# Optimization experiments

Measured on AMD Instinct MI355X. Metric: run time of the kernel, lower is better.

Reference implementation:

```python
import jax, jax.numpy as jnp
import numpy as np

B, T, NH, EX, VOCAB, NLAYER = 8, 510, 12, 768, 256, 6
NBLK = 2 * NLAYER - 1          # 11 blocks, all with out=ex
NE = T + 2                     # CustomEmb output dim = n_embd = 512
HD = EX // NH
EXIT_SCALE = 1.0 / float(np.sqrt(4 * NBLK))  # torch init divides 'exit' params by sqrt(#exit params)


def _ln(x, s, b):
    m = jnp.mean(x, axis=-1, keepdims=True)
    v = jnp.mean((x - m) ** 2, axis=-1, keepdims=True)
    return (x - m) * jax.lax.rsqrt(v + 1e-5) * s + b


def setup_inputs() -> dict:
    key = jax.random.key(0)
    ks = iter(jax.random.split(key, 40))
    def n(shape, scale=0.02):
        return jax.random.normal(next(ks), shape, jnp.float32) * scale
    inp = {}
    inp['idx'] = jax.random.randint(next(ks), (B, T), 0, 2)
    inp['lin_w'] = n((NE, EX)); inp['lin_b'] = n((EX,))
    # stacked per-block params (leading dim NBLK), torch Linear math y = x @ W + b with W stored (in,out)
    inp['ln1_s'] = jnp.ones((NBLK, EX), jnp.float32); inp['ln1_b'] = jnp.zeros((NBLK, EX), jnp.float32)
    inp['qw'] = n((NBLK, EX, EX)); inp['qb'] = n((NBLK, EX))
    inp['kw'] = n((NBLK, EX, EX)); inp['kb'] = n((NBLK, EX))
    inp['vw'] = n((NBLK, EX, EX)); inp['vb'] = n((NBLK, EX))
    inp['ew'] = n((NBLK, EX, EX)) * EXIT_SCALE; inp['eb'] = n((NBLK, EX)) * EXIT_SCALE
    inp['ln2_s'] = jnp.ones((NBLK, EX), jnp.float32); inp['ln2_b'] = jnp.zeros((NBLK, EX), jnp.float32)
    inp['m1w'] = n((NBLK, EX, 4 * EX)); inp['m1b'] = n((NBLK, 4 * EX))
    inp['m2w'] = n((NBLK, 4 * EX, EX)) * EXIT_SCALE; inp['m2b'] = n((NBLK, EX)) * EXIT_SCALE
    inp['lnf_s'] = jnp.ones((EX,), jnp.float32); inp['lnf_b'] = jnp.zeros((EX,), jnp.float32)
    inp['head_w'] = n((EX * T, VOCAB)); inp['head_b'] = n((VOCAB,))
    return inp


def reference(idx, lin_w, lin_b, ln1_s, ln1_b, qw, qb, kw, kb, vw, vb, ew, eb,
              ln2_s, ln2_b, m1w, m1b, m2w, m2b, lnf_s, lnf_b, head_w, head_b):
    # CustomEmb: one-hot of binary token + identity positional encoding -> [B,T,T+2]
    e0 = (idx == 0).astype(jnp.float32)
    e1 = (idx == 1).astype(jnp.float32)
    pos = jnp.broadcast_to(jnp.eye(T, dtype=jnp.float32), (B, T, T))
    x = jnp.concatenate([e0[:, :, None], e1[:, :, None], pos], axis=2)
    x = jax.nn.relu(x @ lin_w + lin_b)                       # [B,T,EX]
    mask = jnp.tril(jnp.ones((T, T), bool))
    inv_sqrt_d = 1.0 / float(np.sqrt(HD))

    def block(x, p):
        l1s, l1b, Qw, Qb, Kw, Kb, Vw, Vb, Ew, Eb, l2s, l2b, M1w, M1b, M2w, M2b = p
        h = _ln(x, l1s, l1b)
        q = (h @ Qw + Qb).reshape(B, T, NH, HD)
        k = (h @ Kw + Kb).reshape(B, T, NH, HD)
        v = (h @ Vw + Vb).reshape(B, T, NH, HD)
        att = jnp.einsum('bqhd,bkhd->bhqk', q, k) * inv_sqrt_d
        att = jnp.where(mask, att, -jnp.inf)
        probs = jax.nn.softmax(att, axis=-1)
        y = jnp.einsum('bhqk,bkhd->bqhd', probs, v).reshape(B, T, EX)
        x = x + y @ Ew + Eb
        h2 = _ln(x, l2s, l2b)
        x = x + jax.nn.relu(h2 @ M1w + M1b) @ M2w + M2b      # MLP depth=2: initial+relu+exit
        return x, None

    x, _ = jax.lax.scan(block, x, (ln1_s, ln1_b, qw, qb, kw, kb, vw, vb,
                                   ew, eb, ln2_s, ln2_b, m1w, m1b, m2w, m2b))
    x = _ln(x, lnf_s, lnf_b)
    return x.reshape(B, -1) @ head_w + head_b                # [B, VOCAB]
```

## Files before the change

### kernel.cpp

```cpp
#include <hip/hip_runtime.h>
#include <hip/hip_bf16.h>
#include <math.h>

constexpr int cB = 8, cT = 510, cNH = 12, cEX = 768, cVOC = 256, cNBLK = 11, cHD = 64;
constexpr int cMB = 512;
constexpr int cMP = 4096;
constexpr int cQKV = 3 * cEX;

typedef __attribute__((ext_vector_type(8))) short bf16x8;
typedef __attribute__((ext_vector_type(4))) float f32x4;
using bf16 = __hip_bfloat16;

__device__ inline void gload16(const void* g, void* l) {
    __builtin_amdgcn_global_load_lds((const __attribute__((address_space(1))) unsigned int*)g,
                                     (__attribute__((address_space(3))) unsigned int*)l, 16, 0, 0);
}
__device__ inline short f2bs(float f) {
    bf16 b = __float2bfloat16(f);
    return *reinterpret_cast<short*>(&b);
}

__global__ __launch_bounds__(256) void embed_kernel(
    const int* __restrict__ idx, const float* __restrict__ lin_w,
    const float* __restrict__ lin_b, float* __restrict__ x)
{
    int row = blockIdx.x;
    int b = row >> 9, t = row & 511;
    float* xr = x + (size_t)row * cEX;
    if (t >= cT) {
        for (int j = threadIdx.x; j < cEX; j += 256) xr[j] = 0.0f;
        return;
    }
    int tok = idx[b * cT + t] & 1;
    const float* wt = lin_w + (size_t)tok * cEX;
    const float* wp = lin_w + (size_t)(2 + t) * cEX;
    for (int j = threadIdx.x; j < cEX; j += 256) {
        float val = wt[j] + wp[j] + lin_b[j];
        xr[j] = fmaxf(val, 0.0f);
    }
}

template<typename OUT>
__global__ __launch_bounds__(256) void ln_wave(
    const float* __restrict__ in, const float* __restrict__ s,
    const float* __restrict__ bsh, OUT* __restrict__ out)
{
    const int wid = threadIdx.x >> 6, lane = threadIdx.x & 63;
    const int row = blockIdx.x * 4 + wid;
    const float* xr = in + (size_t)row * cEX;
    float4 v[3];
    float sum = 0.f, sq = 0.f;
#pragma unroll
    for (int p = 0; p < 3; ++p) {
        v[p] = *(const float4*)&xr[p * 256 + lane * 4];
        sum += v[p].x + v[p].y + v[p].z + v[p].w;
        sq  += v[p].x * v[p].x + v[p].y * v[p].y + v[p].z * v[p].z + v[p].w * v[p].w;
    }
#pragma unroll
    for (int off = 1; off < 64; off <<= 1) {
        sum += __shfl_xor(sum, off, 64);
        sq  += __shfl_xor(sq, off, 64);
    }
    float mean = sum * (1.0f / cEX);
    float var = sq * (1.0f / cEX) - mean * mean;
    float rstd = rsqrtf(var + 1e-5f);
    OUT* outr = out + (size_t)row * cEX;
#pragma unroll
    for (int p = 0; p < 3; ++p) {
        int c = p * 256 + lane * 4;
        float4 sv = *(const float4*)&s[c];
        float4 bv = *(const float4*)&bsh[c];
        float o0 = (v[p].x - mean) * rstd * sv.x + bv.x;
        float o1 = (v[p].y - mean) * rstd * sv.y + bv.y;
        float o2 = (v[p].z - mean) * rstd * sv.z + bv.z;
        float o3 = (v[p].w - mean) * rstd * sv.w + bv.w;
        if constexpr (sizeof(OUT) == 2) {
            short4 pk;
            pk.x = f2bs(o0); pk.y = f2bs(o1); pk.z = f2bs(o2); pk.w = f2bs(o3);
            *(short4*)&outr[c] = pk;
        } else {
            *(float4*)&outr[c] = make_float4(o0, o1, o2, o3);
        }
    }
}

__global__ __launch_bounds__(256) void transpose_w(
    const float* __restrict__ W, bf16* __restrict__ WT,
    int K, int N, size_t w_stride, size_t wt_stride, int wt_row_off)
{
    __shared__ float t[32][33];
    const float* Wb = W + (size_t)blockIdx.z * w_stride;
    bf16* WTb = WT + (size_t)blockIdx.z * wt_stride;
    int n0 = blockIdx.x * 32, k0 = blockIdx.y * 32;
    int c = threadIdx.x & 31, ty = threadIdx.x >> 5;
#pragma unroll
    for (int it = 0; it < 4; ++it) {
        int r = ty + it * 8;
        t[r][c] = Wb[(size_t)(k0 + r) * N + n0 + c];
    }
    __syncthreads();
#pragma unroll
    for (int it = 0; it < 4; ++it) {
        int a = ty + it * 8;
        WTb[(size_t)(wt_row_off + n0 + a) * K + k0 + c] = __float2bfloat16(t[c][a]);
    }
}

__global__ __launch_bounds__(256) void concat_bias(
    const float* __restrict__ qb, const float* __restrict__ kb,
    const float* __restrict__ vb, float* __restrict__ qkvb)
{
    int i = blockIdx.x * 256 + threadIdx.x;
    if (i >= cNBLK * cQKV) return;
    int blk = i / cQKV, c = i - blk * cQKV;
    const float* src; int cc = c;
    if (c < cEX)            { src = qb; }
    else if (c < 2 * cEX)   { src = kb; cc = c - cEX; }
    else                    { src = vb; cc = c - 2 * cEX; }
    qkvb[i] = src[(size_t)blk * cEX + cc];
}

template<int FM, int FN, bool RELU, bool RESID, bool OUTBF16, bool VT>
__global__ __launch_bounds__(256) void gemm_mfma(
    const short* __restrict__ A, const short* __restrict__ BT,
    const float* __restrict__ bias, const float* __restrict__ resid,
    void* __restrict__ Cout, short* __restrict__ vTr, int K, int N)
{
    constexpr int BM = FM * 32, BN = FN * 32;
    __shared__ short ldsA[BM * 64];
    __shared__ short ldsB[BN * 64];
    const int tid = threadIdx.x;
    const int lane = tid & 63, wid = tid >> 6;
    const int wm = wid >> 1, wn = wid & 1;
    const int bm = blockIdx.y * BM, bn = blockIdx.x * BN;

    f32x4 acc[FM][FN];
#pragma unroll
    for (int i = 0; i < FM; ++i)
#pragma unroll
        for (int j = 0; j < FN; ++j)
            acc[i][j] = f32x4{0.f, 0.f, 0.f, 0.f};

    constexpr int CA = BM / 32, CB = BN / 32;
    const int li = lane & 15, gk = lane >> 4;

    for (int k0 = 0; k0 < K; k0 += 64) {
#pragma unroll
        for (int i = 0; i < CA; ++i) {
            int s = i * 256 + tid;
            int r = s >> 3, c = s & 7;
            gload16(A + (size_t)(bm + r) * K + k0 + (c ^ (r & 7)) * 8,
                    (char*)ldsA + (size_t)(i * 256 + wid * 64) * 16);
        }
#pragma unroll
        for (int i = 0; i < CB; ++i) {
            int s = i * 256 + tid;
            int r = s >> 3, c = s & 7;
            gload16(BT + (size_t)(bn + r) * K + k0 + (c ^ (r & 7)) * 8,
                    (char*)ldsB + (size_t)(i * 256 + wid * 64) * 16);
        }
        __syncthreads();

        bf16x8 af[FM][2], bf_[FN][2];
#pragma unroll
        for (int mi = 0; mi < FM; ++mi) {
            int row = wm * FM * 16 + mi * 16 + li;
#pragma unroll
            for (int ks = 0; ks < 2; ++ks)
                af[mi][ks] = *(const bf16x8*)&ldsA[row * 64 + ((ks * 4 + gk) ^ (row & 7)) * 8];
        }
#pragma unroll
        for (int ni = 0; ni < FN; ++ni) {
            int row = wn * FN * 16 + ni * 16 + li;
#pragma unroll
            for (int ks = 0; ks < 2; ++ks)
                bf_[ni][ks] = *(const bf16x8*)&ldsB[row * 64 + ((ks * 4 + gk) ^ (row & 7)) * 8];
        }
#pragma unroll
        for (int ks = 0; ks < 2; ++ks)
#pragma unroll
            for (int mi = 0; mi < FM; ++mi)
#pragma unroll
                for (int ni = 0; ni < FN; ++ni)
                    acc[mi][ni] = __builtin_amdgcn_mfma_f32_16x16x32_bf16(
                        af[mi][ks], bf_[ni][ks], acc[mi][ni], 0, 0, 0);
        __syncthreads();
    }

#pragma unroll
    for (int mi = 0; mi < FM; ++mi) {
#pragma unroll
        for (int ni = 0; ni < FN; ++ni) {
            int col = bn + wn * FN * 16 + ni * 16 + li;
            float bv = bias[col];
            int row0 = bm + wm * FM * 16 + mi * 16 + gk * 4;
            if (VT && col >= 2 * cEX) {
                short4 pk;
                pk.x = f2bs(acc[mi][ni][0] + bv);
                pk.y = f2bs(acc[mi][ni][1] + bv);
                pk.z = f2bs(acc[mi][ni][2] + bv);
                pk.w = f2bs(acc[mi][ni][3] + bv);
                *(short4*)&vTr[(size_t)(col - 2 * cEX) * cMP + row0] = pk;
            } else {
#pragma unroll
                for (int j = 0; j < 4; ++j) {
                    int row = row0 + j;
                    float v = acc[mi][ni][j] + bv;
                    if (RELU) v = fmaxf(v, 0.0f);
                    if (RESID) v += resid[(size_t)row * N + col];
                    if (OUTBF16)
                        ((bf16*)Cout)[(size_t)row * N + col] = __float2bfloat16(v);
                    else
                        ((float*)Cout)[(size_t)row * N + col] = v;
                }
            }
        }
    }
}

__global__ __launch_bounds__(256) void attn_mfma(
    const short* __restrict__ qkv, const short* __restrict__ vT, bf16* __restrict__ y)
{
    const int qt = blockIdx.x, h = blockIdx.y, b = blockIdx.z;
    __shared__ short Ks[32 * 64];
    __shared__ short Vs[64 * 32];
    __shared__ short Ss[4][16][40];
    const int tid = threadIdx.x;
    const int lane = tid & 63, wid = tid >> 6;
    const int li = lane & 15, gk = lane >> 4;

    const size_t rowb = (size_t)b * cMB;
    int qr = qt * 64 + wid * 16 + li;
    int qrc = qr < cT ? qr : cT - 1;
    const short* qrow = qkv + (rowb + qrc) * cQKV + h * cHD;
    bf16x8 qf0 = *(const bf16x8*)(qrow + gk * 8);
    bf16x8 qf1 = *(const bf16x8*)(qrow + 32 + gk * 8);

    f32x4 o[4];
    float mrow[4], lrow[4];
#pragma unroll
    for (int dt = 0; dt < 4; ++dt) o[dt] = f32x4{0.f, 0.f, 0.f, 0.f};
#pragma unroll
    for (int j = 0; j < 4; ++j) { mrow[j] = -3e38f; lrow[j] = 0.f; }

    const int kkey = tid >> 3, kclog = (tid & 7) ^ (kkey & 7);
    const int vd = tid >> 2,  vclog = (tid & 3) ^ (vd & 3);
    const int qloc = qt * 64 + wid * 16 + gk * 4;

    const int nkt = 2 * qt + 2;
    for (int kt = 0; kt < nkt; ++kt) {
        gload16(qkv + (rowb + kt * 32 + kkey) * cQKV + cEX + h * cHD + kclog * 8,
                (char*)Ks + wid * 1024);
        gload16(vT + (size_t)(h * cHD + vd) * cMP + rowb + kt * 32 + vclog * 8,
                (char*)Vs + wid * 1024);
        __syncthreads();

        f32x4 s0 = f32x4{0.f, 0.f, 0.f, 0.f}, s1 = f32x4{0.f, 0.f, 0.f, 0.f};
        {
            int key0 = li, key1 = 16 + li;
            bf16x8 k00 = *(const bf16x8*)&Ks[key0 * 64 + ((0 + gk) ^ (key0 & 7)) * 8];
            bf16x8 k01 = *(const bf16x8*)&Ks[key0 * 64 + ((4 + gk) ^ (key0 & 7)) * 8];
            bf16x8 k10 = *(const bf16x8*)&Ks[key1 * 64 + ((0 + gk) ^ (key1 & 7)) * 8];
            bf16x8 k11 = *(const bf16x8*)&Ks[key1 * 64 + ((4 + gk) ^ (key1 & 7)) * 8];
            s0 = __builtin_amdgcn_mfma_f32_16x16x32_bf16(qf0, k00, s0, 0, 0, 0);
            s0 = __builtin_amdgcn_mfma_f32_16x16x32_bf16(qf1, k01, s0, 0, 0, 0);
            s1 = __builtin_amdgcn_mfma_f32_16x16x32_bf16(qf0, k10, s1, 0, 0, 0);
            s1 = __builtin_amdgcn_mfma_f32_16x16x32_bf16(qf1, k11, s1, 0, 0, 0);
        }

        float sc0[4], sc1[4];
#pragma unroll
        for (int j = 0; j < 4; ++j) {
            int q = qloc + j;
            int key0 = kt * 32 + li, key1 = key0 + 16;
            sc0[j] = (key0 <= q) ? s0[j] * 0.125f : -3e38f;
            sc1[j] = (key1 <= q) ? s1[j] * 0.125f : -3e38f;
        }
        float p0[4], p1[4];
#pragma unroll
        for (int j = 0; j < 4; ++j) {
            float tm = fmaxf(sc0[j], sc1[j]);
            tm = fmaxf(tm, __shfl_xor(tm, 1, 16));
            tm = fmaxf(tm, __shfl_xor(tm, 2, 16));
            tm = fmaxf(tm, __shfl_xor(tm, 4, 16));
            tm = fmaxf(tm, __shfl_xor(tm, 8, 16));
            float mnew = fmaxf(mrow[j], tm);
            p0[j] = __expf(sc0[j] - mnew);
            p1[j] = __expf(sc1[j] - mnew);
            float ps = p0[j] + p1[j];
            ps += __shfl_xor(ps, 1, 16);
            ps += __shfl_xor(ps, 2, 16);
            ps += __shfl_xor(ps, 4, 16);
            ps += __shfl_xor(ps, 8, 16);
            float scale = __expf(mrow[j] - mnew);
            lrow[j] = lrow[j] * scale + ps;
            mrow[j] = mnew;
#pragma unroll
            for (int dt = 0; dt < 4; ++dt) o[dt][j] *= scale;
        }
#pragma unroll
        for (int j = 0; j < 4; ++j) {
            Ss[wid][gk * 4 + j][li]      = f2bs(p0[j]);
            Ss[wid][gk * 4 + j][16 + li] = f2bs(p1[j]);
        }
        bf16x8 pa = *(const bf16x8*)&Ss[wid][li][gk * 8];
#pragma unroll
        for (int dt = 0; dt < 4; ++dt) {
            int d = dt * 16 + li;
            bf16x8 vf = *(const bf16x8*)&Vs[d * 32 + (gk ^ (d & 3)) * 8];
            o[dt] = __builtin_amdgcn_mfma_f32_16x16x32_bf16(pa, vf, o[dt], 0, 0, 0);
        }
        __syncthreads();
    }

#pragma unroll
    for (int j = 0; j < 4; ++j) {
        int q = qloc + j;
        if (q >= cT) continue;
        float inv = 1.0f / lrow[j];
        bf16* yr = y + (rowb + q) * cEX + h * cHD;
#pragma unroll
        for (int dt = 0; dt < 4; ++dt)
            yr[dt * 16 + li] = __float2bfloat16(o[dt][j] * inv);
    }
}

__global__ __launch_bounds__(256) void head_part_kernel(
    const float* __restrict__ xf, const float* __restrict__ hw, float* __restrict__ part)
{
    __shared__ float xs[8][1536];
    const int tid = threadIdx.x;
    const int k0 = blockIdx.x * 1536;
    for (int i = tid; i < 8 * 1536; i += 256) {
        int bb = i / 1536, kk = i - bb * 1536;
        xs[bb][kk] = xf[(size_t)bb * (cMB * cEX) + k0 + kk];
    }
    __syncthreads();
    float acc[8] = {};
    const float* wp = hw + (size_t)k0 * cVOC + tid;
    for (int kk = 0; kk < 1536; ++kk) {
        float w = wp[(size_t)kk * cVOC];
#pragma unroll
        for (int bb = 0; bb < 8; ++bb) acc[bb] += xs[bb][kk] * w;
    }
#pragma unroll
    for (int bb = 0; bb < 8; ++bb)
        part[((size_t)blockIdx.x * 8 + bb) * cVOC + tid] = acc[bb];
}

__global__ __launch_bounds__(256) void head_reduce_kernel(
    const float* __restrict__ part, const float* __restrict__ hb, float* __restrict__ out)
{
    int i = blockIdx.x * 256 + threadIdx.x;
    int bb = i >> 8, vv = i & 255;
    float acc = hb[vv];
    for (int c = 0; c < 255; ++c) acc += part[((size_t)c * 8 + bb) * 256 + vv];
    out[i] = acc;
}

extern "C" void kernel_launch(void* const* d_in, const int* in_sizes, int n_in,
                              void* d_out, int out_size, void* d_ws, size_t ws_size,
                              hipStream_t stream) {
    (void)in_sizes; (void)n_in; (void)out_size; (void)ws_size;
    const int*   idx    = (const int*)d_in[0];
    const float* lin_w  = (const float*)d_in[1];
    const float* lin_b  = (const float*)d_in[2];
    const float* ln1_s  = (const float*)d_in[3];
    const float* ln1_b  = (const float*)d_in[4];
    const float* qw     = (const float*)d_in[5];
    const float* qbias  = (const float*)d_in[6];
    const float* kw     = (const float*)d_in[7];
    const float* kbias  = (const float*)d_in[8];
    const float* vw     = (const float*)d_in[9];
    const float* vbias  = (const float*)d_in[10];
    const float* ew     = (const float*)d_in[11];
    const float* ebias  = (const float*)d_in[12];
    const float* ln2_s  = (const float*)d_in[13];
    const float* ln2_b  = (const float*)d_in[14];
    const float* m1w    = (const float*)d_in[15];
    const float* m1b    = (const float*)d_in[16];
    const float* m2w    = (const float*)d_in[17];
    const float* m2b    = (const float*)d_in[18];
    const float* lnf_s  = (const float*)d_in[19];
    const float* lnf_b  = (const float*)d_in[20];
    const float* head_w = (const float*)d_in[21];
    const float* head_b = (const float*)d_in[22];
    float* out = (float*)d_out;

    const size_t act = (size_t)cMP * cEX;
    float* x    = (float*)d_ws;
    float* xf   = x + act;
    float* part = xf + act;
    float* qkvb = part + 255 * 8 * 256;
    short* qkv  = (short*)(qkvb + cNBLK * cQKV);
    short* vTr  = qkv + (size_t)cMP * cQKV;
    short* h    = vTr + (size_t)cEX * cMP;
    short* h2   = h + act;
    short* y    = h2 + act;
    short* u    = y + act;
    short* wqkvT = u + (size_t)cMP * 4 * cEX;
    short* weT   = wqkvT + (size_t)cNBLK * cQKV * cEX;
    short* wm1T  = weT + (size_t)cNBLK * cEX * cEX;
    short* wm2T  = wm1T + (size_t)cNBLK * cEX * 4 * cEX;

    transpose_w<<<dim3(24, 24, cNBLK), 256, 0, stream>>>(qw, (bf16*)wqkvT, cEX, cEX,
        (size_t)cEX * cEX, (size_t)cQKV * cEX, 0);
    transpose_w<<<dim3(24, 24, cNBLK), 256, 0, stream>>>(kw, (bf16*)wqkvT, cEX, cEX,
        (size_t)cEX * cEX, (size_t)cQKV * cEX, cEX);
    transpose_w<<<dim3(24, 24, cNBLK), 256, 0, stream>>>(vw, (bf16*)wqkvT, cEX, cEX,
        (size_t)cEX * cEX, (size_t)cQKV * cEX, 2 * cEX);
    transpose_w<<<dim3(24, 24, cNBLK), 256, 0, stream>>>(ew, (bf16*)weT, cEX, cEX,
        (size_t)cEX * cEX, (size_t)cEX * cEX, 0);
    transpose_w<<<dim3(96, 24, cNBLK), 256, 0, stream>>>(m1w, (bf16*)wm1T, cEX, 4 * cEX,
        (size_t)cEX * 4 * cEX, (size_t)cEX * 4 * cEX, 0);
    transpose_w<<<dim3(24, 96, cNBLK), 256, 0, stream>>>(m2w, (bf16*)wm2T, 4 * cEX, cEX,
        (size_t)cEX * 4 * cEX, (size_t)cEX * 4 * cEX, 0);
    concat_bias<<<(cNBLK * cQKV + 255) / 256, 256, 0, stream>>>(qbias, kbias, vbias, qkvb);

    embed_kernel<<<cMP, 256, 0, stream>>>(idx, lin_w, lin_b, x);

    for (int blk = 0; blk < cNBLK; ++blk) {
        size_t bo = (size_t)blk * cEX;
        ln_wave<bf16><<<cMP / 4, 256, 0, stream>>>(x, ln1_s + bo, ln1_b + bo, (bf16*)h);
        gemm_mfma<4, 4, false, false, true, true><<<dim3(cQKV / 128, cMP / 128), 256, 0, stream>>>(
            h, wqkvT + (size_t)blk * cQKV * cEX, qkvb + (size_t)blk * cQKV, nullptr,
            qkv, vTr, cEX, cQKV);
        attn_mfma<<<dim3(8, cNH, cB), 256, 0, stream>>>(qkv, vTr, (bf16*)y);
        gemm_mfma<2, 4, false, true, false, false><<<dim3(cEX / 128, cMP / 64), 256, 0, stream>>>(
            y, weT + (size_t)blk * cEX * cEX, ebias + bo, x, x, nullptr, cEX, cEX);
        ln_wave<bf16><<<cMP / 4, 256, 0, stream>>>(x, ln2_s + bo, ln2_b + bo, (bf16*)h2);
        gemm_mfma<4, 4, true, false, true, false><<<dim3(4 * cEX / 128, cMP / 128), 256, 0, stream>>>(
            h2, wm1T + (size_t)blk * cEX * 4 * cEX, m1b + (size_t)blk * 4 * cEX, nullptr,
            u, nullptr, cEX, 4 * cEX);
        gemm_mfma<2, 4, false, true, false, false><<<dim3(cEX / 128, cMP / 64), 256, 0, stream>>>(
            u, wm2T + (size_t)blk * cEX * 4 * cEX, m2b + bo, x, x, nullptr, 4 * cEX, cEX);
    }
    ln_wave<float><<<cMP / 4, 256, 0, stream>>>(x, lnf_s, lnf_b, xf);
    head_part_kernel<<<255, 256, 0, stream>>>(xf, head_w, part);
    head_reduce_kernel<<<8, 256, 0, stream>>>(part, head_b, out);
}
```

Baseline: 2.043 ms.

## Double-buffer LDS tiles in MFMA GEMM with async prefetch two stages ahead

Replaces the single-buffered GEMM main loop with a two-stage LDS ping-pong. The next K-tile's global_load_lds is issued while the current tile is being computed, and partial vmcnt waits replace the full syncthreads drain, so memory latency can overlap MFMA work. It also raises wave priority around the MFMA block with s_setprio. The cost is double the LDS footprint per workgroup, which may reduce occupancy. The hand-set vmcnt counts depend on how many loads each thread issues per stage and must stay in sync with that number.

```diff
diff --git a/kernel.cpp b/kernel.cpp
--- a/kernel.cpp
+++ b/kernel.cpp
@@ -121,18 +121,21 @@
 }
 
 template<int FM, int FN, bool RELU, bool RESID, bool OUTBF16, bool VT>
-__global__ __launch_bounds__(256) void gemm_mfma(
+__global__ __launch_bounds__(256) void gemm_db(
     const short* __restrict__ A, const short* __restrict__ BT,
     const float* __restrict__ bias, const float* __restrict__ resid,
     void* __restrict__ Cout, short* __restrict__ vTr, int K, int N)
 {
     constexpr int BM = FM * 32, BN = FN * 32;
-    __shared__ short ldsA[BM * 64];
-    __shared__ short ldsB[BN * 64];
+    constexpr int TS = (BM + BN) * 64;
+    constexpr int CA = BM / 32, CB = BN / 32;
+    constexpr int LPT = CA + CB;
+    __shared__ short lds[2 * TS];
     const int tid = threadIdx.x;
     const int lane = tid & 63, wid = tid >> 6;
     const int wm = wid >> 1, wn = wid & 1;
     const int bm = blockIdx.y * BM, bn = blockIdx.x * BN;
+    const int li = lane & 15, gk = lane >> 4;
 
     f32x4 acc[FM][FN];
 #pragma unroll
@@ -141,41 +144,56 @@
         for (int j = 0; j < FN; ++j)
             acc[i][j] = f32x4{0.f, 0.f, 0.f, 0.f};
 
-    constexpr int CA = BM / 32, CB = BN / 32;
-    const int li = lane & 15, gk = lane >> 4;
-
-    for (int k0 = 0; k0 < K; k0 += 64) {
+    auto stage = [&](int kt, int buf) {
+        short* la = &lds[buf * TS];
+        short* lb = la + BM * 64;
 #pragma unroll
         for (int i = 0; i < CA; ++i) {
             int s = i * 256 + tid;
             int r = s >> 3, c = s & 7;
-            gload16(A + (size_t)(bm + r) * K + k0 + (c ^ (r & 7)) * 8,
-                    (char*)ldsA + (size_t)(i * 256 + wid * 64) * 16);
+            gload16(A + (size_t)(bm + r) * K + kt * 64 + (c ^ (r & 7)) * 8,
+                    (char*)la + (size_t)(i * 256 + wid * 64) * 16);
         }
 #pragma unroll
         for (int i = 0; i < CB; ++i) {
             int s = i * 256 + tid;
             int r = s >> 3, c = s & 7;
-            gload16(BT + (size_t)(bn + r) * K + k0 + (c ^ (r & 7)) * 8,
-                    (char*)ldsB + (size_t)(i * 256 + wid * 64) * 16);
-        }
-        __syncthreads();
-
+            gload16(BT + (size_t)(bn + r) * K + kt * 64 + (c ^ (r & 7)) * 8,
+                    (char*)lb + (size_t)(i * 256 + wid * 64) * 16);
+        }
+    };
+
+    const int nkt = K >> 6;
+    stage(0, 0);
+    stage(1, 1);
+
+    for (int t = 0; t < nkt; ++t) {
+        if (t + 1 < nkt) {
+            if constexpr (LPT == 8) asm volatile("s_waitcnt vmcnt(8)" ::: "memory");
+            else                    asm volatile("s_waitcnt vmcnt(6)" ::: "memory");
+        } else {
+            asm volatile("s_waitcnt vmcnt(0)" ::: "memory");
+        }
+        __builtin_amdgcn_s_barrier();
+
+        const short* la = &lds[(t & 1) * TS];
+        const short* lb = la + BM * 64;
         bf16x8 af[FM][2], bf_[FN][2];
 #pragma unroll
         for (int mi = 0; mi < FM; ++mi) {
             int row = wm * FM * 16 + mi * 16 + li;
 #pragma unroll
             for (int ks = 0; ks < 2; ++ks)
-                af[mi][ks] = *(const bf16x8*)&ldsA[row * 64 + ((ks * 4 + gk) ^ (row & 7)) * 8];
+                af[mi][ks] = *(const bf16x8*)&la[row * 64 + ((ks * 4 + gk) ^ (row & 7)) * 8];
         }
 #pragma unroll
         for (int ni = 0; ni < FN; ++ni) {
             int row = wn * FN * 16 + ni * 16 + li;
 #pragma unroll
             for (int ks = 0; ks < 2; ++ks)
-                bf_[ni][ks] = *(const bf16x8*)&ldsB[row * 64 + ((ks * 4 + gk) ^ (row & 7)) * 8];
-        }
+                bf_[ni][ks] = *(const bf16x8*)&lb[row * 64 + ((ks * 4 + gk) ^ (row & 7)) * 8];
+        }
+        __builtin_amdgcn_s_setprio(1);
 #pragma unroll
         for (int ks = 0; ks < 2; ++ks)
 #pragma unroll
@@ -184,7 +202,11 @@
                 for (int ni = 0; ni < FN; ++ni)
                     acc[mi][ni] = __builtin_amdgcn_mfma_f32_16x16x32_bf16(
                         af[mi][ks], bf_[ni][ks], acc[mi][ni], 0, 0, 0);
-        __syncthreads();
+        __builtin_amdgcn_s_setprio(0);
+
+        asm volatile("" ::: "memory");
+        __builtin_amdgcn_s_barrier();
+        if (t + 2 < nkt) stage(t + 2, t & 1);
     }
 
 #pragma unroll
@@ -422,17 +444,17 @@
     for (int blk = 0; blk < cNBLK; ++blk) {
         size_t bo = (size_t)blk * cEX;
         ln_wave<bf16><<<cMP / 4, 256, 0, stream>>>(x, ln1_s + bo, ln1_b + bo, (bf16*)h);
-        gemm_mfma<4, 4, false, false, true, true><<<dim3(cQKV / 128, cMP / 128), 256, 0, stream>>>(
+        gemm_db<4, 4, false, false, true, true><<<dim3(cQKV / 128, cMP / 128), 256, 0, stream>>>(
             h, wqkvT + (size_t)blk * cQKV * cEX, qkvb + (size_t)blk * cQKV, nullptr,
             qkv, vTr, cEX, cQKV);
         attn_mfma<<<dim3(8, cNH, cB), 256, 0, stream>>>(qkv, vTr, (bf16*)y);
-        gemm_mfma<2, 4, false, true, false, false><<<dim3(cEX / 128, cMP / 64), 256, 0, stream>>>(
+        gemm_db<2, 4, false, true, false, false><<<dim3(cEX / 128, cMP / 64), 256, 0, stream>>>(
             y, weT + (size_t)blk * cEX * cEX, ebias + bo, x, x, nullptr, cEX, cEX);
         ln_wave<bf16><<<cMP / 4, 256, 0, stream>>>(x, ln2_s + bo, ln2_b + bo, (bf16*)h2);
-        gemm_mfma<4, 4, true, false, true, false><<<dim3(4 * cEX / 128, cMP / 128), 256, 0, stream>>>(
+        gemm_db<4, 4, true, false, true, false><<<dim3(4 * cEX / 128, cMP / 128), 256, 0, stream>>>(
             h2, wm1T + (size_t)blk * cEX * 4 * cEX, m1b + (size_t)blk * 4 * cEX, nullptr,
             u, nullptr, cEX, 4 * cEX);
-        gemm_mfma<2, 4, false, true, false, false><<<dim3(cEX / 128, cMP / 64), 256, 0, stream>>>(
+        gemm_db<2, 4, false, true, false, false><<<dim3(cEX / 128, cMP / 64), 256, 0, stream>>>(
             u, wm2T + (size_t)blk * cEX * 4 * cEX, m2b + bo, x, x, nullptr, 4 * cEX, cEX);
     }
     ln_wave<float><<<cMP / 4, 256, 0, stream>>>(x, lnf_s, lnf_b, xf);
```

After: 1.889 ms. 1.08x faster.
